# Kernel tuning notes

Measured on AMD Instinct MI355X. Metric: run time of the kernel, lower is better.

Reference implementation:

```python
import jax, jax.numpy as jnp
import numpy as np

NUM_AGENTS = 64
IN_FEATURES = 512
OUT_FEATURES = 512
BATCH = 2048


def setup_inputs() -> dict:
    key = jax.random.key(0)
    k1, k2, k3, k4 = jax.random.split(key, 4)
    which_agents = jax.random.randint(k1, (BATCH,), 0, NUM_AGENTS, dtype=jnp.int64 if jax.config.jax_enable_x64 else jnp.int32)
    x = jax.random.normal(k2, (BATCH, IN_FEATURES), dtype=jnp.float32)
    # kaiming_uniform_(a=sqrt(5)) -> bound = sqrt(6 / ((1 + 5) * fan_in)) = 1/sqrt(fan_in)
    bound_w = 1.0 / np.sqrt(IN_FEATURES)
    weight = jax.random.uniform(k3, (NUM_AGENTS, OUT_FEATURES, IN_FEATURES), jnp.float32, -bound_w, bound_w)
    bound_b = 1.0 / np.sqrt(IN_FEATURES)
    bias = jax.random.uniform(k4, (NUM_AGENTS, OUT_FEATURES), jnp.float32, -bound_b, bound_b)
    return {"which_agents": which_agents, "input": x, "weight": weight, "bias": bias}


def reference(which_agents, input, weight, bias):
    # weight[which_agents]: [B, out, in]; batched matvec with input [B, in]
    w = weight[which_agents]          # [B, O, I]
    b = bias[which_agents]            # [B, O]
    return jnp.einsum('boi,bi->bo', w, input) + b
```

## Files before the change

kernel.cpp:

```cpp
#include <hip/hip_runtime.h>


constexpr int BATCH  = 2048;
constexpr int NAGENT = 64;
constexpr int IN_F   = 512;
constexpr int OUT_F  = 512;

constexpr int BN  = 128;
constexpr int MCH = 64;
constexpr int XS  = IN_F + 8;

typedef __attribute__((ext_vector_type(8))) short short8;
typedef __attribute__((ext_vector_type(4))) float f32x4;
typedef __attribute__((ext_vector_type(4))) unsigned int u32x4;
typedef __bf16 bf16x2 __attribute__((ext_vector_type(2)));

__device__ inline unsigned pk_bf(float lo, float hi) {
  bf16x2 v;
  v[0] = (__bf16)lo;
  v[1] = (__bf16)hi;
  return __builtin_bit_cast(unsigned, v);
}

__global__ __launch_bounds__(1024, 4) void agent_linear_mfma4(
    const int*   __restrict__ which,
    const float* __restrict__ x,
    const float* __restrict__ weight,
    const float* __restrict__ bias,
    float*       __restrict__ out) {
  const int tid   = threadIdx.x;
  const int lane  = tid & 63;
  const int wid   = tid >> 6;
  const int w8    = wid & 7;
  const int kh    = wid >> 3;

  const int bid   = blockIdx.x;
  const int agent = (bid & 7) | ((bid >> 5) << 3);
  const int obase = ((bid >> 3) & 3) * BN;

  __shared__ int rowlist_s[BATCH];
  __shared__ int wsum_s[16];
  __shared__ __align__(16) unsigned short Xs[MCH * XS];
  __shared__ float Rs[8][MCH][17];

  const int nl = lane & 15;
  const int kq = lane >> 4;

  const float* wp = weight + ((size_t)(agent * OUT_F + obase + w8 * 16 + nl)) * IN_F
                  + kh * 256 + kq * 8;

  float4 pa[3], pb[3];
#pragma unroll
  for (int j = 0; j < 3; ++j) {
    pa[j] = *(const float4*)(wp + j * 32);
    pb[j] = *(const float4*)(wp + j * 32 + 4);
  }

  const float bv = bias[agent * OUT_F + obase + w8 * 16 + nl];

  int2 v = ((const int2*)which)[tid];
  int lc = (v.x == agent) + (v.y == agent);
  int s = lc;
#pragma unroll
  for (int off = 1; off < 64; off <<= 1) {
    int t = __shfl_up(s, off);
    if (lane >= off) s += t;
  }
  if (lane == 63) wsum_s[wid] = s;
  __syncthreads();
  int base = 0, count = 0;
#pragma unroll
  for (int w = 0; w < 16; ++w) {
    int ws = wsum_s[w];
    if (w < wid) base += ws;
    count += ws;
  }
  {
    int pos = base + s - lc;
    if (v.x == agent) rowlist_s[pos++] = 2 * tid;
    if (v.y == agent) rowlist_s[pos]   = 2 * tid + 1;
  }
  __syncthreads();

  for (int m0 = 0; m0 < count; m0 += MCH) {
    const int mcount = min(MCH, count - m0);
    const int nfrag  = (mcount + 15) >> 4;

#pragma unroll
    for (int t = 0; t < 8; ++t) {
      int idx = t * 1024 + tid;
      int r   = idx >> 7;
      int c4  = idx & 127;
      if (r < mcount) {
        float4 xv = *(const float4*)(x + (size_t)rowlist_s[m0 + r] * IN_F + c4 * 4);
        uint2 w2;
        w2.x = pk_bf(xv.x, xv.y);
        w2.y = pk_bf(xv.z, xv.w);
        *(uint2*)&Xs[r * XS + c4 * 4] = w2;
      }
    }
    __syncthreads();

    f32x4 acc[4] = {{0.f,0.f,0.f,0.f},{0.f,0.f,0.f,0.f},
                    {0.f,0.f,0.f,0.f},{0.f,0.f,0.f,0.f}};
    const int kbase = kh * 256;
#pragma unroll
    for (int k = 0; k < 8; ++k) {
      float4 c0 = pa[k % 3], c1 = pb[k % 3];
      if (k + 3 < 8) {
        pa[k % 3] = *(const float4*)(wp + (k + 3) * 32);
        pb[k % 3] = *(const float4*)(wp + (k + 3) * 32 + 4);
      }
      u32x4 q;
      q[0] = pk_bf(c0.x, c0.y); q[1] = pk_bf(c0.z, c0.w);
      q[2] = pk_bf(c1.x, c1.y); q[3] = pk_bf(c1.z, c1.w);
      short8 bfr = __builtin_bit_cast(short8, q);
#pragma unroll
      for (int i = 0; i < 4; ++i) {
        if (i < nfrag) {
          short8 af = *(const short8*)&Xs[(i * 16 + nl) * XS + kbase + k * 32 + kq * 8];
          acc[i] = __builtin_amdgcn_mfma_f32_16x16x32_bf16(af, bfr, acc[i], 0, 0, 0);
        }
      }
    }

    if (kh == 1) {
#pragma unroll
      for (int i = 0; i < 4; ++i)
        if (i < nfrag)
#pragma unroll
          for (int r = 0; r < 4; ++r)
            Rs[w8][i * 16 + kq * 4 + r][nl] = acc[i][r];
    }
    __syncthreads();

    if (kh == 0) {
#pragma unroll
      for (int i = 0; i < 4; ++i) {
        if (i < nfrag) {
#pragma unroll
          for (int r = 0; r < 4; ++r) {
            int m = i * 16 + kq * 4 + r;
            if (m < mcount) {
              out[(size_t)rowlist_s[m0 + m] * OUT_F + obase + w8 * 16 + nl] =
                  acc[i][r] + Rs[w8][m][nl] + bv;
            }
          }
        }
      }
    }

    if (m0 + MCH < count) {
#pragma unroll
      for (int j = 0; j < 3; ++j) {
        pa[j] = *(const float4*)(wp + j * 32);
        pb[j] = *(const float4*)(wp + j * 32 + 4);
      }
    }
  }
}

extern "C" void kernel_launch(void* const* d_in, const int* in_sizes, int n_in,
                              void* d_out, int out_size, void* d_ws, size_t ws_size,
                              hipStream_t stream) {
  const int*   which = (const int*)d_in[0];
  const float* x     = (const float*)d_in[1];
  const float* w     = (const float*)d_in[2];
  const float* b     = (const float*)d_in[3];
  float*       out   = (float*)d_out;

  dim3 grid(OUT_F / BN * NAGENT);
  agent_linear_mfma4<<<grid, dim3(1024), 0, stream>>>(which, x, w, b, out);
}
```

Baseline: 104.4 us.

## Use smaller 256-thread blocks over 64-column tiles and drop the K-split reduction

```diff
diff --git a/kernel.cpp b/kernel.cpp
--- a/kernel.cpp
+++ b/kernel.cpp
@@ -6,7 +6,7 @@
 constexpr int IN_F   = 512;
 constexpr int OUT_F  = 512;
 
-constexpr int BN  = 128;
+constexpr int BN  = 64;
 constexpr int MCH = 64;
 constexpr int XS  = IN_F + 8;
 
@@ -22,44 +22,46 @@
   return __builtin_bit_cast(unsigned, v);
 }
 
-__global__ __launch_bounds__(1024, 4) void agent_linear_mfma4(
+__global__ __launch_bounds__(256, 2) void agent_linear_mfma5(
     const int*   __restrict__ which,
     const float* __restrict__ x,
     const float* __restrict__ weight,
     const float* __restrict__ bias,
     float*       __restrict__ out) {
-  const int tid   = threadIdx.x;
-  const int lane  = tid & 63;
-  const int wid   = tid >> 6;
-  const int w8    = wid & 7;
-  const int kh    = wid >> 3;
+  const int tid  = threadIdx.x;
+  const int lane = tid & 63;
+  const int wid  = tid >> 6;
 
   const int bid   = blockIdx.x;
-  const int agent = (bid & 7) | ((bid >> 5) << 3);
-  const int obase = ((bid >> 3) & 3) * BN;
+  const int agent = (bid & 7) | ((bid >> 6) << 3);
+  const int obase = ((bid >> 3) & 7) * BN;
 
+  __shared__ int wsum_s[4];
   __shared__ int rowlist_s[BATCH];
-  __shared__ int wsum_s[16];
   __shared__ __align__(16) unsigned short Xs[MCH * XS];
-  __shared__ float Rs[8][MCH][17];
 
   const int nl = lane & 15;
   const int kq = lane >> 4;
 
-  const float* wp = weight + ((size_t)(agent * OUT_F + obase + w8 * 16 + nl)) * IN_F
-                  + kh * 256 + kq * 8;
+  const float* wp = weight + ((size_t)(agent * OUT_F + obase + wid * 16 + nl)) * IN_F
+                  + kq * 8;
 
-  float4 pa[3], pb[3];
+  float4 pa[4], pb[4];
 #pragma unroll
-  for (int j = 0; j < 3; ++j) {
+  for (int j = 0; j < 4; ++j) {
     pa[j] = *(const float4*)(wp + j * 32);
     pb[j] = *(const float4*)(wp + j * 32 + 4);
   }
 
-  const float bv = bias[agent * OUT_F + obase + w8 * 16 + nl];
+  const float bv = bias[agent * OUT_F + obase + wid * 16 + nl];
 
-  int2 v = ((const int2*)which)[tid];
-  int lc = (v.x == agent) + (v.y == agent);
+  const int4* w4p = (const int4*)which;
+  int4 v0 = w4p[2 * tid];
+  int4 v1 = w4p[2 * tid + 1];
+  int m0_ = (v0.x == agent), m1_ = (v0.y == agent), m2_ = (v0.z == agent),
+      m3_ = (v0.w == agent), m4_ = (v1.x == agent), m5_ = (v1.y == agent),
+      m6_ = (v1.z == agent), m7_ = (v1.w == agent);
+  int lc = m0_ + m1_ + m2_ + m3_ + m4_ + m5_ + m6_ + m7_;
   int s = lc;
 #pragma unroll
   for (int off = 1; off < 64; off <<= 1) {
@@ -70,46 +72,55 @@
   __syncthreads();
   int base = 0, count = 0;
 #pragma unroll
-  for (int w = 0; w < 16; ++w) {
+  for (int w = 0; w < 4; ++w) {
     int ws = wsum_s[w];
     if (w < wid) base += ws;
     count += ws;
   }
   {
     int pos = base + s - lc;
-    if (v.x == agent) rowlist_s[pos++] = 2 * tid;
-    if (v.y == agent) rowlist_s[pos]   = 2 * tid + 1;
+    int i0 = 8 * tid;
+    if (m0_) rowlist_s[pos++] = i0;
+    if (m1_) rowlist_s[pos++] = i0 + 1;
+    if (m2_) rowlist_s[pos++] = i0 + 2;
+    if (m3_) rowlist_s[pos++] = i0 + 3;
+    if (m4_) rowlist_s[pos++] = i0 + 4;
+    if (m5_) rowlist_s[pos++] = i0 + 5;
+    if (m6_) rowlist_s[pos++] = i0 + 6;
+    if (m7_) rowlist_s[pos]   = i0 + 7;
   }
-  __syncthreads();
 
   for (int m0 = 0; m0 < count; m0 += MCH) {
     const int mcount = min(MCH, count - m0);
     const int nfrag  = (mcount + 15) >> 4;
 
-#pragma unroll
-    for (int t = 0; t < 8; ++t) {
-      int idx = t * 1024 + tid;
-      int r   = idx >> 7;
-      int c4  = idx & 127;
-      if (r < mcount) {
-        float4 xv = *(const float4*)(x + (size_t)rowlist_s[m0 + r] * IN_F + c4 * 4);
-        uint2 w2;
-        w2.x = pk_bf(xv.x, xv.y);
-        w2.y = pk_bf(xv.z, xv.w);
-        *(uint2*)&Xs[r * XS + c4 * 4] = w2;
+    __syncthreads();
+
+    {
+      const int rh = tid >> 7;
+      const int c4 = tid & 127;
+#pragma unroll 4
+      for (int t = 0; 2 * t < mcount; ++t) {
+        int r = 2 * t + rh;
+        if (r < mcount) {
+          float4 xv = *(const float4*)(x + (size_t)rowlist_s[m0 + r] * IN_F + c4 * 4);
+          uint2 w2;
+          w2.x = pk_bf(xv.x, xv.y);
+          w2.y = pk_bf(xv.z, xv.w);
+          *(uint2*)&Xs[r * XS + c4 * 4] = w2;
+        }
       }
     }
     __syncthreads();
 
     f32x4 acc[4] = {{0.f,0.f,0.f,0.f},{0.f,0.f,0.f,0.f},
                     {0.f,0.f,0.f,0.f},{0.f,0.f,0.f,0.f}};
-    const int kbase = kh * 256;
 #pragma unroll
-    for (int k = 0; k < 8; ++k) {
-      float4 c0 = pa[k % 3], c1 = pb[k % 3];
-      if (k + 3 < 8) {
-        pa[k % 3] = *(const float4*)(wp + (k + 3) * 32);
-        pb[k % 3] = *(const float4*)(wp + (k + 3) * 32 + 4);
+    for (int k = 0; k < 16; ++k) {
+      float4 c0 = pa[k & 3], c1 = pb[k & 3];
+      if (k + 4 < 16) {
+        pa[k & 3] = *(const float4*)(wp + (k + 4) * 32);
+        pb[k & 3] = *(const float4*)(wp + (k + 4) * 32 + 4);
       }
       u32x4 q;
       q[0] = pk_bf(c0.x, c0.y); q[1] = pk_bf(c0.z, c0.w);
@@ -118,33 +129,21 @@
 #pragma unroll
       for (int i = 0; i < 4; ++i) {
         if (i < nfrag) {
-          short8 af = *(const short8*)&Xs[(i * 16 + nl) * XS + kbase + k * 32 + kq * 8];
+          short8 af = *(const short8*)&Xs[(i * 16 + nl) * XS + k * 32 + kq * 8];
           acc[i] = __builtin_amdgcn_mfma_f32_16x16x32_bf16(af, bfr, acc[i], 0, 0, 0);
         }
       }
     }
 
-    if (kh == 1) {
 #pragma unroll
-      for (int i = 0; i < 4; ++i)
-        if (i < nfrag)
+    for (int i = 0; i < 4; ++i) {
+      if (i < nfrag) {
 #pragma unroll
-          for (int r = 0; r < 4; ++r)
-            Rs[w8][i * 16 + kq * 4 + r][nl] = acc[i][r];
-    }
-    __syncthreads();
-
-    if (kh == 0) {
-#pragma unroll
-      for (int i = 0; i < 4; ++i) {
-        if (i < nfrag) {
-#pragma unroll
-          for (int r = 0; r < 4; ++r) {
-            int m = i * 16 + kq * 4 + r;
-            if (m < mcount) {
-              out[(size_t)rowlist_s[m0 + m] * OUT_F + obase + w8 * 16 + nl] =
-                  acc[i][r] + Rs[w8][m][nl] + bv;
-            }
+        for (int r = 0; r < 4; ++r) {
+          int m = i * 16 + kq * 4 + r;
+          if (m < mcount) {
+            out[(size_t)rowlist_s[m0 + m] * OUT_F + obase + wid * 16 + nl] =
+                acc[i][r] + bv;
           }
         }
       }
@@ -152,7 +151,7 @@
 
     if (m0 + MCH < count) {
 #pragma unroll
-      for (int j = 0; j < 3; ++j) {
+      for (int j = 0; j < 4; ++j) {
         pa[j] = *(const float4*)(wp + j * 32);
         pb[j] = *(const float4*)(wp + j * 32 + 4);
       }
@@ -170,5 +169,5 @@
   float*       out   = (float*)d_out;
 
   dim3 grid(OUT_F / BN * NAGENT);
-  agent_linear_mfma4<<<grid, dim3(1024), 0, stream>>>(which, x, w, b, out);
+  agent_linear_mfma5<<<grid, dim3(256), 0, stream>>>(which, x, w, b, out);
 }
```

Result: slower. 113.9 us (+9.1%).

## Split X staging into two K-halves and overlap second half load with MFMAs

Applied to the files above, without the earlier changes.

```diff
diff --git a/kernel.cpp b/kernel.cpp
--- a/kernel.cpp
+++ b/kernel.cpp
@@ -22,7 +22,7 @@
   return __builtin_bit_cast(unsigned, v);
 }
 
-__global__ __launch_bounds__(1024, 4) void agent_linear_mfma4(
+__global__ __launch_bounds__(1024, 4) void agent_linear_mfma7(
     const int*   __restrict__ which,
     const float* __restrict__ x,
     const float* __restrict__ weight,
@@ -43,6 +43,8 @@
   __shared__ __align__(16) unsigned short Xs[MCH * XS];
   __shared__ float Rs[8][MCH][17];
 
+  int2 v = ((const int2*)which)[tid];
+
   const int nl = lane & 15;
   const int kq = lane >> 4;
 
@@ -58,7 +60,6 @@
 
   const float bv = bias[agent * OUT_F + obase + w8 * 16 + nl];
 
-  int2 v = ((const int2*)which)[tid];
   int lc = (v.x == agent) + (v.y == agent);
   int s = lc;
 #pragma unroll
@@ -80,32 +81,73 @@
     if (v.x == agent) rowlist_s[pos++] = 2 * tid;
     if (v.y == agent) rowlist_s[pos]   = 2 * tid + 1;
   }
-  __syncthreads();
+
+  const int cA = (lane & 31) + ((lane >> 5) << 6);
+  const int cB = cA + 32;
 
   for (int m0 = 0; m0 < count; m0 += MCH) {
     const int mcount = min(MCH, count - m0);
     const int nfrag  = (mcount + 15) >> 4;
 
-#pragma unroll
-    for (int t = 0; t < 8; ++t) {
-      int idx = t * 1024 + tid;
-      int r   = idx >> 7;
-      int c4  = idx & 127;
+    __syncthreads();
+
+#pragma unroll
+    for (int t = 0; t < 4; ++t) {
+      int r = t * 16 + wid;
       if (r < mcount) {
-        float4 xv = *(const float4*)(x + (size_t)rowlist_s[m0 + r] * IN_F + c4 * 4);
+        float4 xv = *(const float4*)(x + (size_t)rowlist_s[m0 + r] * IN_F + cA * 4);
         uint2 w2;
         w2.x = pk_bf(xv.x, xv.y);
         w2.y = pk_bf(xv.z, xv.w);
-        *(uint2*)&Xs[r * XS + c4 * 4] = w2;
-      }
+        *(uint2*)&Xs[r * XS + cA * 4] = w2;
+      }
+    }
+    float4 sb[4];
+#pragma unroll
+    for (int t = 0; t < 4; ++t) {
+      int r = t * 16 + wid;
+      sb[t] = (r < mcount)
+            ? *(const float4*)(x + (size_t)rowlist_s[m0 + r] * IN_F + cB * 4)
+            : float4{0.f, 0.f, 0.f, 0.f};
     }
     __syncthreads();
 
     f32x4 acc[4] = {{0.f,0.f,0.f,0.f},{0.f,0.f,0.f,0.f},
                     {0.f,0.f,0.f,0.f},{0.f,0.f,0.f,0.f}};
     const int kbase = kh * 256;
-#pragma unroll
-    for (int k = 0; k < 8; ++k) {
+
+#pragma unroll
+    for (int k = 0; k < 4; ++k) {
+      float4 c0 = pa[k % 3], c1 = pb[k % 3];
+      pa[k % 3] = *(const float4*)(wp + (k + 3) * 32);
+      pb[k % 3] = *(const float4*)(wp + (k + 3) * 32 + 4);
+      u32x4 q;
+      q[0] = pk_bf(c0.x, c0.y); q[1] = pk_bf(c0.z, c0.w);
+      q[2] = pk_bf(c1.x, c1.y); q[3] = pk_bf(c1.z, c1.w);
+      short8 bfr = __builtin_bit_cast(short8, q);
+#pragma unroll
+      for (int i = 0; i < 4; ++i) {
+        if (i < nfrag) {
+          short8 af = *(const short8*)&Xs[(i * 16 + nl) * XS + kbase + k * 32 + kq * 8];
+          acc[i] = __builtin_amdgcn_mfma_f32_16x16x32_bf16(af, bfr, acc[i], 0, 0, 0);
+        }
+      }
+    }
+
+#pragma unroll
+    for (int t = 0; t < 4; ++t) {
+      int r = t * 16 + wid;
+      if (r < mcount) {
+        uint2 w2;
+        w2.x = pk_bf(sb[t].x, sb[t].y);
+        w2.y = pk_bf(sb[t].z, sb[t].w);
+        *(uint2*)&Xs[r * XS + cB * 4] = w2;
+      }
+    }
+    __syncthreads();
+
+#pragma unroll
+    for (int k = 4; k < 8; ++k) {
       float4 c0 = pa[k % 3], c1 = pb[k % 3];
       if (k + 3 < 8) {
         pa[k % 3] = *(const float4*)(wp + (k + 3) * 32);
@@ -170,5 +212,5 @@
   float*       out   = (float*)d_out;
 
   dim3 grid(OUT_F / BN * NAGENT);
-  agent_linear_mfma4<<<grid, dim3(1024), 0, stream>>>(which, x, w, b, out);
+  agent_linear_mfma7<<<grid, dim3(1024), 0, stream>>>(which, x, w, b, out);
 }
```

Result: no change. 105.0 us (+0.6%).

## Load gathered input rows directly from global memory instead of staging in LDS

Applied to the files above, without the earlier changes.

```diff
diff --git a/kernel.cpp b/kernel.cpp
--- a/kernel.cpp
+++ b/kernel.cpp
@@ -8,7 +8,6 @@
 
 constexpr int BN  = 128;
 constexpr int MCH = 64;
-constexpr int XS  = IN_F + 8;
 
 typedef __attribute__((ext_vector_type(8))) short short8;
 typedef __attribute__((ext_vector_type(4))) float f32x4;
@@ -22,7 +21,7 @@
   return __builtin_bit_cast(unsigned, v);
 }
 
-__global__ __launch_bounds__(1024, 4) void agent_linear_mfma4(
+__global__ __launch_bounds__(1024, 4) void agent_linear_mfma8(
     const int*   __restrict__ which,
     const float* __restrict__ x,
     const float* __restrict__ weight,
@@ -40,8 +39,9 @@
 
   __shared__ int rowlist_s[BATCH];
   __shared__ int wsum_s[16];
-  __shared__ __align__(16) unsigned short Xs[MCH * XS];
   __shared__ float Rs[8][MCH][17];
+
+  int2 v = ((const int2*)which)[tid];
 
   const int nl = lane & 15;
   const int kq = lane >> 4;
@@ -58,7 +58,6 @@
 
   const float bv = bias[agent * OUT_F + obase + w8 * 16 + nl];
 
-  int2 v = ((const int2*)which)[tid];
   int lc = (v.x == agent) + (v.y == agent);
   int s = lc;
 #pragma unroll
@@ -80,30 +79,23 @@
     if (v.x == agent) rowlist_s[pos++] = 2 * tid;
     if (v.y == agent) rowlist_s[pos]   = 2 * tid + 1;
   }
-  __syncthreads();
 
   for (int m0 = 0; m0 < count; m0 += MCH) {
     const int mcount = min(MCH, count - m0);
     const int nfrag  = (mcount + 15) >> 4;
 
+    __syncthreads();
+
+    const float* xp[4];
 #pragma unroll
-    for (int t = 0; t < 8; ++t) {
-      int idx = t * 1024 + tid;
-      int r   = idx >> 7;
-      int c4  = idx & 127;
-      if (r < mcount) {
-        float4 xv = *(const float4*)(x + (size_t)rowlist_s[m0 + r] * IN_F + c4 * 4);
-        uint2 w2;
-        w2.x = pk_bf(xv.x, xv.y);
-        w2.y = pk_bf(xv.z, xv.w);
-        *(uint2*)&Xs[r * XS + c4 * 4] = w2;
-      }
+    for (int i = 0; i < 4; ++i) {
+      int m  = i * 16 + nl;
+      int mm = (m < mcount) ? m : 0;
+      xp[i] = x + (size_t)rowlist_s[m0 + mm] * IN_F + kh * 256 + kq * 8;
     }
-    __syncthreads();
 
     f32x4 acc[4] = {{0.f,0.f,0.f,0.f},{0.f,0.f,0.f,0.f},
                     {0.f,0.f,0.f,0.f},{0.f,0.f,0.f,0.f}};
-    const int kbase = kh * 256;
 #pragma unroll
     for (int k = 0; k < 8; ++k) {
       float4 c0 = pa[k % 3], c1 = pb[k % 3];
@@ -118,7 +110,12 @@
 #pragma unroll
       for (int i = 0; i < 4; ++i) {
         if (i < nfrag) {
-          short8 af = *(const short8*)&Xs[(i * 16 + nl) * XS + kbase + k * 32 + kq * 8];
+          float4 a0 = *(const float4*)(xp[i] + k * 32);
+          float4 a1 = *(const float4*)(xp[i] + k * 32 + 4);
+          u32x4 qa;
+          qa[0] = pk_bf(a0.x, a0.y); qa[1] = pk_bf(a0.z, a0.w);
+          qa[2] = pk_bf(a1.x, a1.y); qa[3] = pk_bf(a1.z, a1.w);
+          short8 af = __builtin_bit_cast(short8, qa);
           acc[i] = __builtin_amdgcn_mfma_f32_16x16x32_bf16(af, bfr, acc[i], 0, 0, 0);
         }
       }
@@ -170,5 +167,5 @@
   float*       out   = (float*)d_out;
 
   dim3 grid(OUT_F / BN * NAGENT);
-  agent_linear_mfma4<<<grid, dim3(1024), 0, stream>>>(which, x, w, b, out);
+  agent_linear_mfma8<<<grid, dim3(1024), 0, stream>>>(which, x, w, b, out);
 }
```

New measurement: 122.8 us. +17.7%, slower.
